# Performance work log

Hardware: AMD Instinct MI355X
Metric: run time of the kernel (lower is better)

The kernel has to match this reference:

```python
import jax, jax.numpy as jnp
import numpy as np

D_MODEL = 2048
NUM_Q_HEADS = 16
NUM_KV_HEADS = 4
HEAD_DIM = D_MODEL // NUM_Q_HEADS  # 128
NUM_GROUPS = NUM_Q_HEADS // NUM_KV_HEADS  # 4
ROPE_BASE = 10000.0


def _rope_cos_sin(seq_len, head_dim):
    inv_freq = 1.0 / (ROPE_BASE ** (jnp.arange(0, head_dim, 2, dtype=jnp.float32) / head_dim))
    t = jnp.arange(seq_len, dtype=jnp.float32)
    freqs = jnp.outer(t, inv_freq)            # [S, head_dim/2]
    emb = jnp.concatenate([freqs, freqs], -1)  # [S, head_dim]
    return jnp.cos(emb)[None, :, None, :], jnp.sin(emb)[None, :, None, :]


def _rotate_half(x):
    half = x.shape[-1] // 2
    return jnp.concatenate([-x[..., half:], x[..., :half]], axis=-1)


def setup_inputs() -> dict:
    key = jax.random.key(0)
    k0, k1, k2, k3, k4 = jax.random.split(key, 5)
    B, S = 2, 2048
    kv_dim = HEAD_DIM * NUM_KV_HEADS
    scale = D_MODEL ** -0.5
    return {
        "x": jax.random.normal(k0, (B, S, D_MODEL), jnp.float32),
        "attention_mask": jnp.ones((B, S), jnp.int32),
        "Wq": jax.random.normal(k1, (D_MODEL, D_MODEL), jnp.float32) * scale,
        "Wk": jax.random.normal(k2, (D_MODEL, kv_dim), jnp.float32) * scale,
        "Wv": jax.random.normal(k3, (D_MODEL, kv_dim), jnp.float32) * scale,
        "Wo": jax.random.normal(k4, (D_MODEL, D_MODEL), jnp.float32) * scale,
    }


def reference(x, attention_mask, Wq, Wk, Wv, Wo):
    B, S, _ = x.shape
    q = (x @ Wq).reshape(B, S, NUM_Q_HEADS, HEAD_DIM)
    k = (x @ Wk).reshape(B, S, NUM_KV_HEADS, HEAD_DIM)
    v = (x @ Wv).reshape(B, S, NUM_KV_HEADS, HEAD_DIM)

    cos, sin = _rope_cos_sin(S, HEAD_DIM)  # [1,S,1,hd]
    q = q * cos + _rotate_half(q) * sin
    k = k * cos + _rotate_half(k) * sin

    # [B, H, S, hd]; replicate KV heads across groups (repeat_interleave)
    q = q.transpose(0, 2, 1, 3)
    k = jnp.repeat(k.transpose(0, 2, 1, 3), NUM_GROUPS, axis=1)
    v = jnp.repeat(v.transpose(0, 2, 1, 3), NUM_GROUPS, axis=1)

    scale = HEAD_DIM ** -0.5
    scores = jnp.einsum("bhqd,bhkd->bhqk", q, k) * scale
    mask = attention_mask[:, None, None, :]  # [B,1,1,S] over keys
    scores = jnp.where(mask == 0, jnp.float32(-jnp.inf), scores)
    probs = jax.nn.softmax(scores, axis=-1)
    out = jnp.einsum("bhqk,bhkd->bhqd", probs, v)
    out = out.transpose(0, 2, 1, 3).reshape(B, S, D_MODEL)
    return out @ Wo
```

## Files before the change

### kernel.cpp

```cpp
#include <hip/hip_runtime.h>
#include <hip/hip_bf16.h>

typedef __attribute__((ext_vector_type(4))) float f32x4;
typedef __attribute__((ext_vector_type(8))) short s16x8;
typedef __attribute__((ext_vector_type(4))) short s16x4;

__device__ __forceinline__ float fexp2(float x) {
    float y; asm("v_exp_f32 %0, %1" : "=v"(y) : "v"(x)); return y;
}

__global__ void rope_tables(float* __restrict__ cosT, float* __restrict__ sinT) {
    const int s = blockIdx.x, j = threadIdx.x;
    const double inv = pow(10000.0, -(double)j / 64.0);
    const double f = (double)s * inv;
    cosT[s * 64 + j] = (float)cos(f);
    sinT[s * 64 + j] = (float)sin(f);
}

__global__ void mask_bias(const int* __restrict__ mask, float* __restrict__ mb, int n) {
    const int i = blockIdx.x * 256 + threadIdx.x;
    if (i < n) mb[i] = (mask[i] == 0) ? -1e30f : 0.f;
}

__global__ __launch_bounds__(256)
void cast_f32_bf16(const float* __restrict__ src, __hip_bfloat16* __restrict__ dst, int n4) {
    const int i = blockIdx.x * 256 + threadIdx.x;
    if (i < n4) {
        f32x4 v = *reinterpret_cast<const f32x4*>(src + (size_t)i * 4);
        union { s16x4 v4; __hip_bfloat16 h[4]; } u;
#pragma unroll
        for (int j = 0; j < 4; ++j) u.h[j] = __float2bfloat16(v[j]);
        *reinterpret_cast<s16x4*>(dst + (size_t)i * 4) = u.v4;
    }
}

__global__ __launch_bounds__(256)
void transpose_cast(const float* __restrict__ src, __hip_bfloat16* __restrict__ dst,
                    int R, int C) {
    __shared__ __align__(16) float t[32][33];
    const int tx = threadIdx.x, ty = threadIdx.y;
    const int r0 = blockIdx.y * 32, c0 = blockIdx.x * 32;
#pragma unroll
    for (int i = 0; i < 32; i += 8)
        t[ty + i][tx] = src[(size_t)(r0 + ty + i) * C + c0 + tx];
    __syncthreads();
#pragma unroll
    for (int i = 0; i < 32; i += 8)
        dst[(size_t)(c0 + ty + i) * R + r0 + tx] = __float2bfloat16(t[tx][ty + i]);
}

__global__ __launch_bounds__(256)
void vt_transpose(const __hip_bfloat16* __restrict__ qkv, __hip_bfloat16* __restrict__ Vt) {
    __shared__ unsigned short t[32][33];
    const int tx = threadIdx.x, ty = threadIdx.y;
    const int s0 = blockIdx.x * 32, d0 = blockIdx.y * 32;
    const int bh = blockIdx.z, b = bh >> 2, hh = bh & 3;
    const unsigned short* q = (const unsigned short*)qkv;
#pragma unroll
    for (int i = 0; i < 32; i += 8)
        t[ty + i][tx] = q[(size_t)(b * 2048 + s0 + ty + i) * 3072 + 2560 + hh * 128 + d0 + tx];
    __syncthreads();
#pragma unroll
    for (int i = 0; i < 32; i += 8)
        ((unsigned short*)Vt)[((size_t)(bh * 128) + d0 + ty + i) * 2048 + s0 + tx] = t[tx][ty + i];
}

template<int NI, bool BF16OUT>
__global__ __launch_bounds__(512, 1)
void gemm256_bt(const __hip_bfloat16* __restrict__ A,
                const __hip_bfloat16* __restrict__ Bt,
                void* __restrict__ Cv, int M, int N, int K, int NX) {
    constexpr int NB = NI / 2;
    __shared__ __align__(16) __hip_bfloat16 sm[4][2][8192];
    const int tid = threadIdx.x;
    const int l = tid & 63, w = tid >> 6;
    const int lo = l & 15, hi = l >> 4;
    const int wm = w >> 2, wn = w & 3;
    const int id = blockIdx.x, slot = id >> 3;
    const int by = (id & 7) * 2 + slot / NX;
    const int bx = slot % NX;
    const int row0 = by * 256;
    const int col0 = bx * (NI * 64);
    const int nk = K >> 5;

    f32x4 acc[8][NI];
#pragma unroll
    for (int mi = 0; mi < 8; ++mi)
#pragma unroll
        for (int ni = 0; ni < NI; ++ni) acc[mi][ni] = f32x4{0.f, 0.f, 0.f, 0.f};

    auto stage = [&](int kt) {
        const int s = kt & 3, k0 = kt << 5;
#pragma unroll
        for (int i = 0; i < 2; ++i) {
            const int c = i * 512 + tid;
            const int r = c >> 2, sw = ((c & 3) ^ ((r >> 1) & 3)) * 8;
            __builtin_amdgcn_global_load_lds(
                (const __attribute__((address_space(1))) void*)(A + (size_t)(row0 + r) * K + k0 + sw),
                (__attribute__((address_space(3))) void*)(&sm[s][0][c * 8]), 16, 0, 0);
        }
#pragma unroll
        for (int i = 0; i < NB; ++i) {
            const int c = i * 512 + tid;
            const int r = c >> 2, sw = ((c & 3) ^ ((r >> 1) & 3)) * 8;
            __builtin_amdgcn_global_load_lds(
                (const __attribute__((address_space(1))) void*)(Bt + (size_t)(col0 + r) * K + k0 + sw),
                (__attribute__((address_space(3))) void*)(&sm[s][1][c * 8]), 16, 0, 0);
        }
    };

    stage(0); stage(1); stage(2);
    for (int kt = 0; kt < nk; ++kt) {
        const int s = kt & 3;
        if (kt < nk - 2) {
            if constexpr (NI == 4) asm volatile("s_waitcnt vmcnt(8)" ::: "memory");
            else                   asm volatile("s_waitcnt vmcnt(6)" ::: "memory");
        } else if (kt == nk - 2) {
            if constexpr (NI == 4) asm volatile("s_waitcnt vmcnt(4)" ::: "memory");
            else                   asm volatile("s_waitcnt vmcnt(3)" ::: "memory");
        } else {
            asm volatile("s_waitcnt vmcnt(0)" ::: "memory");
        }
        asm volatile("s_waitcnt lgkmcnt(0)" ::: "memory");
        asm volatile("s_barrier" ::: "memory");
        if (kt + 3 < nk) stage(kt + 3);

        s16x8 af[8], bf[NI];
        const int rsw = ((lo >> 1) & 3);
#pragma unroll
        for (int mi = 0; mi < 8; ++mi)
            af[mi] = *reinterpret_cast<const s16x8*>(
                &sm[s][0][(wm * 128 + mi * 16 + lo) * 32 + ((hi ^ rsw) * 8)]);
#pragma unroll
        for (int ni = 0; ni < NI; ++ni)
            bf[ni] = *reinterpret_cast<const s16x8*>(
                &sm[s][1][(wn * NI * 16 + ni * 16 + lo) * 32 + ((hi ^ rsw) * 8)]);
        __builtin_amdgcn_s_setprio(1);
#pragma unroll
        for (int mi = 0; mi < 8; ++mi)
#pragma unroll
            for (int ni = 0; ni < NI; ++ni)
                acc[mi][ni] = __builtin_amdgcn_mfma_f32_16x16x32_bf16(af[mi], bf[ni], acc[mi][ni], 0, 0, 0);
        __builtin_amdgcn_s_setprio(0);
    }
    const int rbase = row0 + wm * 128 + hi * 4;
    const int cbase = col0 + wn * NI * 16 + lo;
    if constexpr (BF16OUT) {
        __hip_bfloat16* C = (__hip_bfloat16*)Cv;
#pragma unroll
        for (int mi = 0; mi < 8; ++mi)
#pragma unroll
            for (int ni = 0; ni < NI; ++ni)
#pragma unroll
                for (int r = 0; r < 4; ++r)
                    C[(size_t)(rbase + mi * 16 + r) * N + cbase + ni * 16] =
                        __float2bfloat16(acc[mi][ni][r]);
    } else {
        float* C = (float*)Cv;
#pragma unroll
        for (int mi = 0; mi < 8; ++mi)
#pragma unroll
            for (int ni = 0; ni < NI; ++ni)
#pragma unroll
                for (int r = 0; r < 4; ++r)
                    C[(size_t)(rbase + mi * 16 + r) * N + cbase + ni * 16] = acc[mi][ni][r];
    }
}

__global__ __launch_bounds__(256)
void rope_scatter(const __hip_bfloat16* __restrict__ qkv,
                  const float* __restrict__ cosT, const float* __restrict__ sinT,
                  __hip_bfloat16* __restrict__ Qr, __hip_bfloat16* __restrict__ Kr) {
    const int m = blockIdx.y;
    const int col4 = blockIdx.x * 256 + threadIdx.x;
    if (col4 >= 640) return;
    const int col = col4 * 4;
    const int b = m >> 11, s = m & 2047;
    const int d = col & 127;
    const int j = d & 63;
    union { s16x4 v4; __hip_bfloat16 h[4]; } vv, pp, u;
    vv.v4 = *reinterpret_cast<const s16x4*>(qkv + (size_t)m * 3072 + col);
    pp.v4 = *reinterpret_cast<const s16x4*>(qkv + (size_t)m * 3072 + (col ^ 64));
    const f32x4 c4 = *reinterpret_cast<const f32x4*>(cosT + s * 64 + j);
    const f32x4 s4 = *reinterpret_cast<const f32x4*>(sinT + s * 64 + j);
    const float sgn = (d < 64) ? -1.f : 1.f;
#pragma unroll
    for (int i = 0; i < 4; ++i)
        u.h[i] = __float2bfloat16(__bfloat162float(vv.h[i]) * c4[i] +
                                  sgn * __bfloat162float(pp.h[i]) * s4[i]);
    if (col < 2048) {
        const int hh = col >> 7;
        *reinterpret_cast<s16x4*>(&Qr[((size_t)(b * 16 + hh) * 2048 + s) * 128 + d]) = u.v4;
    } else {
        const int hh = (col - 2048) >> 7;
        *reinterpret_cast<s16x4*>(&Kr[((size_t)(b * 4 + hh) * 2048 + s) * 128 + d]) = u.v4;
    }
}

__global__ __launch_bounds__(512, 4)
void attn_kernel(const __hip_bfloat16* __restrict__ Qr,
                 const __hip_bfloat16* __restrict__ Kr,
                 const __hip_bfloat16* __restrict__ Vt,
                 const float* __restrict__ maskb,
                 __hip_bfloat16* __restrict__ Oo) {
    const int S = 2048;
    const int qt = blockIdx.x;
    const int bh = blockIdx.y;
    const int b = bh >> 4, h = bh & 15, kvh = h >> 2;
    const int tid = threadIdx.x;
    const int l = tid & 63, w = tid >> 6;
    const int lo = l & 15, hi = l >> 4;
    __shared__ __align__(16) __hip_bfloat16 Ks[2][64 * 128];
    __shared__ __align__(16) __hip_bfloat16 Vs[2][128 * 64];
    __shared__ __align__(16) __hip_bfloat16 Ps[8][16 * 64];

    const __hip_bfloat16* Qb = Qr + (size_t)(b * 16 + h) * S * 128;
    const __hip_bfloat16* Kb = Kr + (size_t)(b * 4 + kvh) * S * 128;
    const __hip_bfloat16* Vb = Vt + (size_t)(b * 4 + kvh) * 128 * S;
    const float* mrow = maskb + b * S;

    const int qrow = qt * 128 + w * 16 + lo;
    s16x8 qf[4];
#pragma unroll
    for (int kc = 0; kc < 4; ++kc)
        qf[kc] = *reinterpret_cast<const s16x8*>(Qb + (size_t)qrow * 128 + kc * 32 + hi * 8);

    float m_run = -1e30f, l_run = 0.f;
    f32x4 o[8];
#pragma unroll
    for (int n = 0; n < 8; ++n) o[n] = f32x4{0.f, 0.f, 0.f, 0.f};
    const float scale2 = 0.12751682f;

    const int krow = tid >> 4, kc8 = tid & 15;
    const int koff = (kc8 ^ (krow & 7)) * 8;
    const int vrow = tid >> 3, vc8 = tid & 7;
    const int voff = (vc8 ^ (vrow & 7)) * 8;

    s16x8 kreg[2], vreg[2];
    auto load_tile = [&](int kv0) {
#pragma unroll
        for (int i = 0; i < 2; ++i)
            kreg[i] = *reinterpret_cast<const s16x8*>(
                Kb + (size_t)(kv0 + i * 32 + krow) * 128 + kc8 * 8);
#pragma unroll
        for (int i = 0; i < 2; ++i)
            vreg[i] = *reinterpret_cast<const s16x8*>(
                Vb + (size_t)(i * 64 + vrow) * S + kv0 + vc8 * 8);
    };

    auto body = [&](int kt, __hip_bfloat16* Kc, __hip_bfloat16* Vc) {
        const int kv0 = kt * 64;
        f32x4 bi[4];
#pragma unroll
        for (int ksub = 0; ksub < 4; ++ksub)
            bi[ksub] = *reinterpret_cast<const f32x4*>(mrow + kv0 + ksub * 16 + hi * 4);
#pragma unroll
        for (int i = 0; i < 2; ++i)
            *reinterpret_cast<s16x8*>(Kc + (i * 32 + krow) * 128 + koff) = kreg[i];
#pragma unroll
        for (int i = 0; i < 2; ++i)
            *reinterpret_cast<s16x8*>(Vc + (i * 64 + vrow) * 64 + voff) = vreg[i];
        if (kt < 31) load_tile(kv0 + 64);
        __syncthreads();

        f32x4 sc[4] = {};
        __builtin_amdgcn_s_setprio(1);
#pragma unroll
        for (int ksub = 0; ksub < 4; ++ksub) {
            const int kr = ksub * 16 + lo;
            const int ksw = kr & 7;
#pragma unroll
            for (int kc = 0; kc < 4; ++kc) {
                s16x8 kf = *reinterpret_cast<const s16x8*>(
                    Kc + kr * 128 + (((kc * 4 + hi) ^ ksw) * 8));
                sc[ksub] = __builtin_amdgcn_mfma_f32_16x16x32_bf16(kf, qf[kc], sc[ksub], 0, 0, 0);
            }
        }
        __builtin_amdgcn_s_setprio(0);
#pragma unroll
        for (int ksub = 0; ksub < 4; ++ksub)
#pragma unroll
            for (int r = 0; r < 4; ++r)
                sc[ksub][r] = fmaf(sc[ksub][r], scale2, bi[ksub][r]);
        float a0 = fmaxf(fmaxf(sc[0][0], sc[0][1]), fmaxf(sc[0][2], sc[0][3]));
        float a1 = fmaxf(fmaxf(sc[1][0], sc[1][1]), fmaxf(sc[1][2], sc[1][3]));
        float a2 = fmaxf(fmaxf(sc[2][0], sc[2][1]), fmaxf(sc[2][2], sc[2][3]));
        float a3 = fmaxf(fmaxf(sc[3][0], sc[3][1]), fmaxf(sc[3][2], sc[3][3]));
        float mx = fmaxf(fmaxf(a0, a1), fmaxf(a2, a3));
        mx = fmaxf(mx, __shfl_xor(mx, 16));
        mx = fmaxf(mx, __shfl_xor(mx, 32));
        if (__ballot(mx > m_run + 11.5417f) != 0ull) {
            const float mnew = fmaxf(m_run, mx);
            const float alpha = fexp2(m_run - mnew);
            m_run = mnew;
            l_run *= alpha;
            float ar[4];
#pragma unroll
            for (int r = 0; r < 4; ++r) ar[r] = __shfl(alpha, hi * 4 + r);
#pragma unroll
            for (int n = 0; n < 8; ++n)
#pragma unroll
                for (int r = 0; r < 4; ++r) o[n][r] *= ar[r];
        }
        float s0 = 0.f, s1 = 0.f, s2 = 0.f, s3 = 0.f;
#pragma unroll
        for (int r = 0; r < 4; ++r) {
            sc[0][r] = fexp2(sc[0][r] - m_run); s0 += sc[0][r];
            sc[1][r] = fexp2(sc[1][r] - m_run); s1 += sc[1][r];
            sc[2][r] = fexp2(sc[2][r] - m_run); s2 += sc[2][r];
            sc[3][r] = fexp2(sc[3][r] - m_run); s3 += sc[3][r];
        }
        float ssum = (s0 + s1) + (s2 + s3);
        ssum += __shfl_xor(ssum, 16);
        ssum += __shfl_xor(ssum, 32);
        l_run += ssum;
        __hip_bfloat16* pb = &Ps[w][0];
#pragma unroll
        for (int ksub = 0; ksub < 4; ++ksub) {
            unsigned int d0, d1;
            asm("v_cvt_pk_bf16_f32 %0, %1, %2" : "=v"(d0) : "v"(sc[ksub][0]), "v"(sc[ksub][1]));
            asm("v_cvt_pk_bf16_f32 %0, %1, %2" : "=v"(d1) : "v"(sc[ksub][2]), "v"(sc[ksub][3]));
            const int byteoff = lo * 128 + (((ksub * 2 + (hi >> 1)) ^ (lo & 7)) * 16) + (hi & 1) * 8;
            uint2 dd; dd.x = d0; dd.y = d1;
            *reinterpret_cast<uint2*>(reinterpret_cast<char*>(pb) + byteoff) = dd;
        }
        __builtin_amdgcn_s_setprio(1);
#pragma unroll
        for (int kg = 0; kg < 2; ++kg) {
            s16x8 pa = *reinterpret_cast<const s16x8*>(
                pb + lo * 64 + (((kg * 4 + hi) ^ (lo & 7)) * 8));
#pragma unroll
            for (int n = 0; n < 8; ++n) {
                const int vr = n * 16 + lo;
                s16x8 vb = *reinterpret_cast<const s16x8*>(
                    Vc + vr * 64 + (((kg * 4 + hi) ^ (vr & 7)) * 8));
                o[n] = __builtin_amdgcn_mfma_f32_16x16x32_bf16(pa, vb, o[n], 0, 0, 0);
            }
        }
        __builtin_amdgcn_s_setprio(0);
    };

    load_tile(0);
    for (int kt2 = 0; kt2 < 16; ++kt2) {
        body(2 * kt2,     &Ks[0][0], &Vs[0][0]);
        body(2 * kt2 + 1, &Ks[1][0], &Vs[1][0]);
    }
    float lr[4];
#pragma unroll
    for (int r = 0; r < 4; ++r) lr[r] = __shfl(l_run, hi * 4 + r);
    const int orow = b * S + qt * 128 + w * 16 + (hi * 4);
    const int ocol = h * 128 + lo;
#pragma unroll
    for (int n = 0; n < 8; ++n)
#pragma unroll
        for (int r = 0; r < 4; ++r)
            Oo[(size_t)(orow + r) * 2048 + ocol + n * 16] = __float2bfloat16(o[n][r] / lr[r]);
}

extern "C" void kernel_launch(void* const* d_in, const int* in_sizes, int n_in,
                              void* d_out, int out_size, void* d_ws, size_t ws_size,
                              hipStream_t stream) {
    const float* x  = (const float*)d_in[0];
    const int* mask = (const int*)d_in[1];
    const float* Wq = (const float*)d_in[2];
    const float* Wk = (const float*)d_in[3];
    const float* Wv = (const float*)d_in[4];
    const float* Wo = (const float*)d_in[5];
    float* out = (float*)d_out;

    char* ws = (char*)d_ws;
    size_t off = 0;
    auto alloc = [&](size_t bytes) -> void* {
        void* p = ws + off;
        off += (bytes + 255) & ~(size_t)255;
        return p;
    };
    __hip_bfloat16* xb     = (__hip_bfloat16*)alloc(4096ULL * 2048 * 2);
    __hip_bfloat16* wqkv_t = (__hip_bfloat16*)alloc(3072ULL * 2048 * 2);
    __hip_bfloat16* wo_t   = (__hip_bfloat16*)alloc(2048ULL * 2048 * 2);
    __hip_bfloat16* qkvb   = (__hip_bfloat16*)alloc(4096ULL * 3072 * 2);
    __hip_bfloat16* Kr     = (__hip_bfloat16*)alloc(2ULL * 4 * 2048 * 128 * 2);
    __hip_bfloat16* Vt     = (__hip_bfloat16*)alloc(2ULL * 4 * 2048 * 128 * 2);
    float*          cosT   = (float*)alloc(2048ULL * 64 * 4);
    float*          sinT   = (float*)alloc(2048ULL * 64 * 4);
    float*          maskb  = (float*)alloc(2ULL * 2048 * 4);
    __hip_bfloat16* attno  = (__hip_bfloat16*)alloc(4096ULL * 2048 * 2);
    __hip_bfloat16* Qr    = xb;

    rope_tables<<<dim3(2048), dim3(64), 0, stream>>>(cosT, sinT);
    mask_bias<<<dim3(16), dim3(256), 0, stream>>>(mask, maskb, 4096);
    cast_f32_bf16<<<dim3(8192), dim3(256), 0, stream>>>(x, xb, 2097152);
    transpose_cast<<<dim3(64, 64), dim3(32, 8), 0, stream>>>(Wq, wqkv_t, 2048, 2048);
    transpose_cast<<<dim3(16, 64), dim3(32, 8), 0, stream>>>(Wk, wqkv_t + 2048ULL * 2048, 2048, 512);
    transpose_cast<<<dim3(16, 64), dim3(32, 8), 0, stream>>>(Wv, wqkv_t + 2560ULL * 2048, 2048, 512);
    transpose_cast<<<dim3(64, 64), dim3(32, 8), 0, stream>>>(Wo, wo_t, 2048, 2048);

    gemm256_bt<4, true><<<dim3(192), dim3(512), 0, stream>>>(xb, wqkv_t, qkvb, 4096, 3072, 2048, 12);
    rope_scatter<<<dim3(3, 4096), dim3(256), 0, stream>>>(qkvb, cosT, sinT, Qr, Kr);
    vt_transpose<<<dim3(64, 4, 8), dim3(32, 8), 0, stream>>>(qkvb, Vt);
    attn_kernel<<<dim3(16, 32), dim3(512), 0, stream>>>(Qr, Kr, Vt, maskb, attno);
    gemm256_bt<2, false><<<dim3(256), dim3(512), 0, stream>>>(attno, wo_t, out, 4096, 2048, 2048, 16);
}
```

Baseline: 238.5 us.

## Rewrite attention with 32x32x16 MFMA and register-resident P via permlane32 swap

Reorganizes the attention kernel so each of 4 waves owns 32 query rows, using 32x32x16 bf16 MFMAs for both QK^T and PV instead of 16x16x32. The probability tile is transposed in registers with permlane32_swap rather than round-tripping through LDS, which removes the per-wave P shared buffer and its LDS writes and reads. Row max and sum reductions now need only one cross-lane shuffle, and the exp is computed against the stale running max with a rescale applied when needed. The trade-offs are larger register footprint per thread (16-wide accumulators), fewer threads per block and lower occupancy per CU, and a manual waitcnt/barrier in place of __syncthreads.

Result: faster. 226.0 us (-5.2%).

```diff
diff --git a/kernel.cpp b/kernel.cpp
--- a/kernel.cpp
+++ b/kernel.cpp
@@ -2,8 +2,10 @@
 #include <hip/hip_bf16.h>
 
 typedef __attribute__((ext_vector_type(4))) float f32x4;
+typedef __attribute__((ext_vector_type(16))) float f32x16;
 typedef __attribute__((ext_vector_type(8))) short s16x8;
 typedef __attribute__((ext_vector_type(4))) short s16x4;
+typedef __attribute__((ext_vector_type(2))) unsigned int u32x2;
 
 __device__ __forceinline__ float fexp2(float x) {
     float y; asm("v_exp_f32 %0, %1" : "=v"(y) : "v"(x)); return y;
@@ -197,7 +199,7 @@
     }
 }
 
-__global__ __launch_bounds__(512, 4)
+__global__ __launch_bounds__(256, 2)
 void attn_kernel(const __hip_bfloat16* __restrict__ Qr,
                  const __hip_bfloat16* __restrict__ Kr,
                  const __hip_bfloat16* __restrict__ Vt,
@@ -208,27 +210,28 @@
     const int bh = blockIdx.y;
     const int b = bh >> 4, h = bh & 15, kvh = h >> 2;
     const int tid = threadIdx.x;
-    const int l = tid & 63, w = tid >> 6;
-    const int lo = l & 15, hi = l >> 4;
+    const int l = tid & 63, wv_ = tid >> 6;
+    const int lq = l & 31, hi2 = l >> 5;
     __shared__ __align__(16) __hip_bfloat16 Ks[2][64 * 128];
     __shared__ __align__(16) __hip_bfloat16 Vs[2][128 * 64];
-    __shared__ __align__(16) __hip_bfloat16 Ps[8][16 * 64];
 
     const __hip_bfloat16* Qb = Qr + (size_t)(b * 16 + h) * S * 128;
     const __hip_bfloat16* Kb = Kr + (size_t)(b * 4 + kvh) * S * 128;
     const __hip_bfloat16* Vb = Vt + (size_t)(b * 4 + kvh) * 128 * S;
     const float* mrow = maskb + b * S;
 
-    const int qrow = qt * 128 + w * 16 + lo;
-    s16x8 qf[4];
-#pragma unroll
-    for (int kc = 0; kc < 4; ++kc)
-        qf[kc] = *reinterpret_cast<const s16x8*>(Qb + (size_t)qrow * 128 + kc * 32 + hi * 8);
-
-    float m_run = -1e30f, l_run = 0.f;
-    f32x4 o[8];
-#pragma unroll
-    for (int n = 0; n < 8; ++n) o[n] = f32x4{0.f, 0.f, 0.f, 0.f};
+    const int qrow = qt * 128 + wv_ * 32 + lq;
+    s16x8 qf[8];
+#pragma unroll
+    for (int ks = 0; ks < 8; ++ks)
+        qf[ks] = *reinterpret_cast<const s16x8*>(Qb + (size_t)qrow * 128 + ks * 16 + hi2 * 8);
+
+    float m_run = 0.f, l_run = 0.f;
+    f32x16 o[4];
+#pragma unroll
+    for (int dt = 0; dt < 4; ++dt)
+#pragma unroll
+        for (int r = 0; r < 16; ++r) o[dt][r] = 0.f;
     const float scale2 = 0.12751682f;
 
     const int krow = tid >> 4, kc8 = tid & 15;
@@ -236,105 +239,113 @@
     const int vrow = tid >> 3, vc8 = tid & 7;
     const int voff = (vc8 ^ (vrow & 7)) * 8;
 
-    s16x8 kreg[2], vreg[2];
+    s16x8 kreg[4], vreg[4];
     auto load_tile = [&](int kv0) {
 #pragma unroll
-        for (int i = 0; i < 2; ++i)
+        for (int i = 0; i < 4; ++i)
             kreg[i] = *reinterpret_cast<const s16x8*>(
-                Kb + (size_t)(kv0 + i * 32 + krow) * 128 + kc8 * 8);
-#pragma unroll
-        for (int i = 0; i < 2; ++i)
+                Kb + (size_t)(kv0 + i * 16 + krow) * 128 + kc8 * 8);
+#pragma unroll
+        for (int i = 0; i < 4; ++i)
             vreg[i] = *reinterpret_cast<const s16x8*>(
-                Vb + (size_t)(i * 64 + vrow) * S + kv0 + vc8 * 8);
+                Vb + (size_t)(i * 32 + vrow) * S + kv0 + vc8 * 8);
     };
 
     auto body = [&](int kt, __hip_bfloat16* Kc, __hip_bfloat16* Vc) {
         const int kv0 = kt * 64;
-        f32x4 bi[4];
-#pragma unroll
-        for (int ksub = 0; ksub < 4; ++ksub)
-            bi[ksub] = *reinterpret_cast<const f32x4*>(mrow + kv0 + ksub * 16 + hi * 4);
-#pragma unroll
-        for (int i = 0; i < 2; ++i)
-            *reinterpret_cast<s16x8*>(Kc + (i * 32 + krow) * 128 + koff) = kreg[i];
-#pragma unroll
-        for (int i = 0; i < 2; ++i)
-            *reinterpret_cast<s16x8*>(Vc + (i * 64 + vrow) * 64 + voff) = vreg[i];
+        f32x4 bi[2][4];
+#pragma unroll
+        for (int sub = 0; sub < 2; ++sub)
+#pragma unroll
+            for (int r4 = 0; r4 < 4; ++r4)
+                bi[sub][r4] = *reinterpret_cast<const f32x4*>(
+                    mrow + kv0 + sub * 32 + r4 * 8 + hi2 * 4);
+#pragma unroll
+        for (int i = 0; i < 4; ++i)
+            *reinterpret_cast<s16x8*>(Kc + (i * 16 + krow) * 128 + koff) = kreg[i];
+#pragma unroll
+        for (int i = 0; i < 4; ++i)
+            *reinterpret_cast<s16x8*>(Vc + (i * 32 + vrow) * 64 + voff) = vreg[i];
         if (kt < 31) load_tile(kv0 + 64);
-        __syncthreads();
-
-        f32x4 sc[4] = {};
+        asm volatile("s_waitcnt lgkmcnt(0)" ::: "memory");
+        asm volatile("s_barrier" ::: "memory");
+
+        f32x16 sc[2];
+#pragma unroll
+        for (int sub = 0; sub < 2; ++sub)
+#pragma unroll
+            for (int r = 0; r < 16; ++r) sc[sub][r] = 0.f;
         __builtin_amdgcn_s_setprio(1);
 #pragma unroll
-        for (int ksub = 0; ksub < 4; ++ksub) {
-            const int kr = ksub * 16 + lo;
+        for (int sub = 0; sub < 2; ++sub) {
+            const int kr = sub * 32 + lq;
             const int ksw = kr & 7;
 #pragma unroll
-            for (int kc = 0; kc < 4; ++kc) {
+            for (int ks = 0; ks < 8; ++ks) {
                 s16x8 kf = *reinterpret_cast<const s16x8*>(
-                    Kc + kr * 128 + (((kc * 4 + hi) ^ ksw) * 8));
-                sc[ksub] = __builtin_amdgcn_mfma_f32_16x16x32_bf16(kf, qf[kc], sc[ksub], 0, 0, 0);
+                    Kc + kr * 128 + (((ks * 2 + hi2) ^ ksw) * 8));
+                sc[sub] = __builtin_amdgcn_mfma_f32_32x32x16_bf16(kf, qf[ks], sc[sub], 0, 0, 0);
             }
         }
         __builtin_amdgcn_s_setprio(0);
 #pragma unroll
-        for (int ksub = 0; ksub < 4; ++ksub)
-#pragma unroll
-            for (int r = 0; r < 4; ++r)
-                sc[ksub][r] = fmaf(sc[ksub][r], scale2, bi[ksub][r]);
-        float a0 = fmaxf(fmaxf(sc[0][0], sc[0][1]), fmaxf(sc[0][2], sc[0][3]));
-        float a1 = fmaxf(fmaxf(sc[1][0], sc[1][1]), fmaxf(sc[1][2], sc[1][3]));
-        float a2 = fmaxf(fmaxf(sc[2][0], sc[2][1]), fmaxf(sc[2][2], sc[2][3]));
-        float a3 = fmaxf(fmaxf(sc[3][0], sc[3][1]), fmaxf(sc[3][2], sc[3][3]));
-        float mx = fmaxf(fmaxf(a0, a1), fmaxf(a2, a3));
-        mx = fmaxf(mx, __shfl_xor(mx, 16));
+        for (int sub = 0; sub < 2; ++sub)
+#pragma unroll
+            for (int r = 0; r < 16; ++r)
+                sc[sub][r] = fmaf(sc[sub][r], scale2, bi[sub][r >> 2][r & 3]);
+        float mx = sc[0][0];
+#pragma unroll
+        for (int sub = 0; sub < 2; ++sub)
+#pragma unroll
+            for (int r = 0; r < 16; ++r) mx = fmaxf(mx, sc[sub][r]);
+        float ss = 0.f;
+#pragma unroll
+        for (int sub = 0; sub < 2; ++sub)
+#pragma unroll
+            for (int r = 0; r < 16; ++r) {
+                sc[sub][r] = fexp2(sc[sub][r] - m_run);
+                ss += sc[sub][r];
+            }
         mx = fmaxf(mx, __shfl_xor(mx, 32));
         if (__ballot(mx > m_run + 11.5417f) != 0ull) {
             const float mnew = fmaxf(m_run, mx);
             const float alpha = fexp2(m_run - mnew);
             m_run = mnew;
             l_run *= alpha;
-            float ar[4];
-#pragma unroll
-            for (int r = 0; r < 4; ++r) ar[r] = __shfl(alpha, hi * 4 + r);
-#pragma unroll
-            for (int n = 0; n < 8; ++n)
-#pragma unroll
-                for (int r = 0; r < 4; ++r) o[n][r] *= ar[r];
-        }
-        float s0 = 0.f, s1 = 0.f, s2 = 0.f, s3 = 0.f;
-#pragma unroll
-        for (int r = 0; r < 4; ++r) {
-            sc[0][r] = fexp2(sc[0][r] - m_run); s0 += sc[0][r];
-            sc[1][r] = fexp2(sc[1][r] - m_run); s1 += sc[1][r];
-            sc[2][r] = fexp2(sc[2][r] - m_run); s2 += sc[2][r];
-            sc[3][r] = fexp2(sc[3][r] - m_run); s3 += sc[3][r];
-        }
-        float ssum = (s0 + s1) + (s2 + s3);
-        ssum += __shfl_xor(ssum, 16);
-        ssum += __shfl_xor(ssum, 32);
-        l_run += ssum;
-        __hip_bfloat16* pb = &Ps[w][0];
-#pragma unroll
-        for (int ksub = 0; ksub < 4; ++ksub) {
-            unsigned int d0, d1;
-            asm("v_cvt_pk_bf16_f32 %0, %1, %2" : "=v"(d0) : "v"(sc[ksub][0]), "v"(sc[ksub][1]));
-            asm("v_cvt_pk_bf16_f32 %0, %1, %2" : "=v"(d1) : "v"(sc[ksub][2]), "v"(sc[ksub][3]));
-            const int byteoff = lo * 128 + (((ksub * 2 + (hi >> 1)) ^ (lo & 7)) * 16) + (hi & 1) * 8;
-            uint2 dd; dd.x = d0; dd.y = d1;
-            *reinterpret_cast<uint2*>(reinterpret_cast<char*>(pb) + byteoff) = dd;
+            ss *= alpha;
+#pragma unroll
+            for (int sub = 0; sub < 2; ++sub)
+#pragma unroll
+                for (int r = 0; r < 16; ++r) sc[sub][r] *= alpha;
+#pragma unroll
+            for (int dt = 0; dt < 4; ++dt)
+#pragma unroll
+                for (int r = 0; r < 16; ++r) o[dt][r] *= alpha;
+        }
+        ss += __shfl_xor(ss, 32);
+        l_run += ss;
+        unsigned int wvp[8][2];
+#pragma unroll
+        for (int g = 0; g < 8; ++g) {
+            const int sub = g >> 2, r4 = g & 3;
+            asm("v_cvt_pk_bf16_f32 %0, %1, %2"
+                : "=v"(wvp[g][0]) : "v"(sc[sub][r4 * 4 + 0]), "v"(sc[sub][r4 * 4 + 1]));
+            asm("v_cvt_pk_bf16_f32 %0, %1, %2"
+                : "=v"(wvp[g][1]) : "v"(sc[sub][r4 * 4 + 2]), "v"(sc[sub][r4 * 4 + 3]));
         }
         __builtin_amdgcn_s_setprio(1);
 #pragma unroll
-        for (int kg = 0; kg < 2; ++kg) {
-            s16x8 pa = *reinterpret_cast<const s16x8*>(
-                pb + lo * 64 + (((kg * 4 + hi) ^ (lo & 7)) * 8));
-#pragma unroll
-            for (int n = 0; n < 8; ++n) {
-                const int vr = n * 16 + lo;
-                s16x8 vb = *reinterpret_cast<const s16x8*>(
-                    Vc + vr * 64 + (((kg * 4 + hi) ^ (vr & 7)) * 8));
-                o[n] = __builtin_amdgcn_mfma_f32_16x16x32_bf16(pa, vb, o[n], 0, 0, 0);
+        for (int ks = 0; ks < 4; ++ks) {
+            u32x2 r0 = __builtin_amdgcn_permlane32_swap(wvp[2 * ks][0], wvp[2 * ks + 1][0], false, false);
+            u32x2 r1 = __builtin_amdgcn_permlane32_swap(wvp[2 * ks][1], wvp[2 * ks + 1][1], false, false);
+            union { unsigned int u[4]; s16x8 v; } pf;
+            pf.u[0] = r0.x; pf.u[1] = r1.x; pf.u[2] = r0.y; pf.u[3] = r1.y;
+#pragma unroll
+            for (int dt = 0; dt < 4; ++dt) {
+                const int dvr = dt * 32 + lq;
+                s16x8 vf = *reinterpret_cast<const s16x8*>(
+                    Vc + dvr * 64 + (((ks * 2 + hi2) ^ (dvr & 7)) * 8));
+                o[dt] = __builtin_amdgcn_mfma_f32_32x32x16_bf16(vf, pf.v, o[dt], 0, 0, 0);
             }
         }
         __builtin_amdgcn_s_setprio(0);
@@ -345,16 +356,18 @@
         body(2 * kt2,     &Ks[0][0], &Vs[0][0]);
         body(2 * kt2 + 1, &Ks[1][0], &Vs[1][0]);
     }
-    float lr[4];
-#pragma unroll
-    for (int r = 0; r < 4; ++r) lr[r] = __shfl(l_run, hi * 4 + r);
-    const int orow = b * S + qt * 128 + w * 16 + (hi * 4);
-    const int ocol = h * 128 + lo;
-#pragma unroll
-    for (int n = 0; n < 8; ++n)
-#pragma unroll
-        for (int r = 0; r < 4; ++r)
-            Oo[(size_t)(orow + r) * 2048 + ocol + n * 16] = __float2bfloat16(o[n][r] / lr[r]);
+    const float inv = 1.f / l_run;
+    const size_t obase = (size_t)(b * S + qt * 128 + wv_ * 32 + lq) * 2048 + h * 128;
+#pragma unroll
+    for (int dt = 0; dt < 4; ++dt)
+#pragma unroll
+        for (int r4 = 0; r4 < 4; ++r4) {
+            union { s16x4 v4; __hip_bfloat16 hh[4]; } u;
+#pragma unroll
+            for (int j = 0; j < 4; ++j)
+                u.hh[j] = __float2bfloat16(o[dt][r4 * 4 + j] * inv);
+            *reinterpret_cast<s16x4*>(&Oo[obase + dt * 32 + r4 * 8 + hi2 * 4]) = u.v4;
+        }
 }
 
 extern "C" void kernel_launch(void* const* d_in, const int* in_sizes, int n_in,
@@ -398,6 +411,6 @@
     gemm256_bt<4, true><<<dim3(192), dim3(512), 0, stream>>>(xb, wqkv_t, qkvb, 4096, 3072, 2048, 12);
     rope_scatter<<<dim3(3, 4096), dim3(256), 0, stream>>>(qkvb, cosT, sinT, Qr, Kr);
     vt_transpose<<<dim3(64, 4, 8), dim3(32, 8), 0, stream>>>(qkvb, Vt);
-    attn_kernel<<<dim3(16, 32), dim3(512), 0, stream>>>(Qr, Kr, Vt, maskb, attno);
+    attn_kernel<<<dim3(16, 32), dim3(256), 0, stream>>>(Qr, Kr, Vt, maskb, attno);
     gemm256_bt<2, false><<<dim3(256), dim3(512), 0, stream>>>(attno, wo_t, out, 4096, 2048, 2048, 16);
 }
```
